# Kernel optimization log

Measured on AMD Instinct MI355X. Metric: run time of the kernel, lower is better.

## Reference

```python
import jax, jax.numpy as jnp
import numpy as np


def setup_inputs() -> dict:
    key = jax.random.key(0)
    ks = jax.random.split(key, 10)
    B, D_X, D_H, D_S, D_T = 16384, 256, 512, 128, 128
    G = 4 * D_H
    sc = lambda d: 1.0 / np.sqrt(d)
    return {
        "x": jax.random.normal(ks[0], (B, D_X), jnp.float32),
        "h": jax.random.normal(ks[1], (B, D_H), jnp.float32),
        "c": jax.random.normal(ks[2], (B, D_H), jnp.float32),
        "spatial_per_step": jax.random.normal(ks[3], (B, D_S), jnp.float32),
        "temporal_per_step": jax.random.normal(ks[4], (B, D_T), jnp.float32),
        "W_x": jax.random.normal(ks[5], (D_X, G), jnp.float32) * sc(D_X),
        "W_h": jax.random.normal(ks[6], (D_H, G), jnp.float32) * sc(D_H),
        "b_h": jax.random.normal(ks[7], (G,), jnp.float32) * 0.01,
        "W_s": jax.random.normal(ks[8], (D_S, G), jnp.float32) * sc(D_S),
        "W_t": jax.random.normal(ks[9], (D_T, G), jnp.float32) * sc(D_T),
    }


def reference(x, h, c, spatial_per_step, temporal_per_step, W_x, W_h, b_h, W_s, W_t):
    H = W_h.shape[0]  # hidden_size
    # Four gate projections summed (the fusion opportunity): [B, 4H]
    preact = (x @ W_x) + (h @ W_h + b_h) + (spatial_per_step @ W_s) + (temporal_per_step @ W_t)
    i_g = jax.nn.sigmoid(preact[:, 0 * H:1 * H])
    f_g = jax.nn.sigmoid(preact[:, 1 * H:2 * H])
    o_g = jax.nn.sigmoid(preact[:, 2 * H:3 * H])
    c_g = jnp.tanh(preact[:, 3 * H:4 * H])
    c_new = f_g * c + i_g * c_g
    # NOTE: faithful to the source, h = tanh(o * c) (not o * tanh(c))
    h_new = jnp.tanh(o_g * c_new)
    return (h_new, c_new)
```

## Files before the change

kernel.cpp:

```cpp
#include <hip/hip_runtime.h>
#include <hip/hip_bf16.h>
#include <cstdint>

#define B_DIM 16384
#define DX 256
#define DH 512
#define DS 128
#define DT 128
#define KDIM 1024
#define NDIM 2048
#define HOUT 512

#define NT 32
#define SLOT 4096

typedef __attribute__((ext_vector_type(8))) short short8;
typedef __attribute__((ext_vector_type(4))) float floatx4;

union bf16x8 {
  short8 v;
  __hip_bfloat16 b[8];
};

__device__ __forceinline__ float fast_sigmoid(float x) {
  return 1.f / (1.f + __expf(-x));
}
__device__ __forceinline__ float fast_tanh(float x) {
  float e = __expf(-2.f * x);
  return (1.f - e) / (1.f + e);
}


__global__ __launch_bounds__(256) void pack_AW(
    const float* __restrict__ x, const float* __restrict__ h,
    const float* __restrict__ s, const float* __restrict__ t,
    const float* __restrict__ Wx, const float* __restrict__ Wh,
    const float* __restrict__ Ws, const float* __restrict__ Wt,
    __hip_bfloat16* __restrict__ Ap, __hip_bfloat16* __restrict__ Wp) {
  const int bid = blockIdx.x;
  if (bid < B_DIM * KDIM / 8 / 256) {
    int tid = bid * 256 + threadIdx.x;
    int r = tid >> 7;
    int k = (tid & 127) * 8;
    const float* p;
    if (k < 768) {
      p = (k < 256) ? (x + (size_t)r * DX + k) : (h + (size_t)r * DH + (k - 256));
    } else {
      p = (k < 896) ? (s + (size_t)r * DS + (k - 768)) : (t + (size_t)r * DT + (k - 896));
    }
    floatx4 v0 = *(const floatx4*)p;
    floatx4 v1 = *(const floatx4*)(p + 4);
    bf16x8 o;
#pragma unroll
    for (int j = 0; j < 4; ++j) {
      o.b[j]     = __float2bfloat16(v0[j]);
      o.b[4 + j] = __float2bfloat16(v1[j]);
    }
    *(short8*)(Ap + (size_t)tid * 8) = o.v;
  } else {
    int tid = (bid - B_DIM * KDIM / 8 / 256) * 256 + threadIdx.x;
    int pcol = tid >> 7;
    int k0 = (tid & 127) * 8;
    int nblk = pcol >> 7, r7 = pcol & 127;
    int wn = r7 >> 6, g = (r7 >> 4) & 3, hl = r7 & 15;
    int col = g * 512 + nblk * 32 + wn * 16 + hl;
    const float* src; int kl;
    if (k0 < 256)      { src = Wx; kl = k0; }
    else if (k0 < 768) { src = Wh; kl = k0 - 256; }
    else if (k0 < 896) { src = Ws; kl = k0 - 768; }
    else               { src = Wt; kl = k0 - 896; }
    bf16x8 o;
#pragma unroll
    for (int rr = 0; rr < 8; ++rr)
      o.b[rr] = __float2bfloat16(src[(size_t)(kl + rr) * NDIM + col]);
    *(short8*)(Wp + (size_t)tid * 8) = o.v;
  }
}

#define GLD(src, dst)                                              \
  __builtin_amdgcn_global_load_lds(                                \
      (const __attribute__((address_space(1))) void*)(src),        \
      (__attribute__((address_space(3))) void*)(dst), 16, 0, 0)

__global__ __launch_bounds__(256, 3) void lstm_gemm(
    const __hip_bfloat16* __restrict__ Ap, const __hip_bfloat16* __restrict__ Wp,
    const float* __restrict__ bh, const float* __restrict__ c_in,
    float* __restrict__ out) {
  __shared__ unsigned short As[3 * SLOT];
  __shared__ unsigned short Bs[3 * SLOT];

  const int tid = threadIdx.x;
  const int lane = tid & 63;
  const int wid = tid >> 6;
  const int wm = wid & 1;
  const int wn = wid >> 1;
  const int q = lane >> 4;
  const int fr = lane & 15;

  const int bid = blockIdx.x;
  const int wg = (bid & 7) * 256 + (bid >> 3);
  const int mb = wg >> 4;
  const int nblk = wg & 15;
  const int m0 = mb * 128;

  int aOff[4], bOff[4];
#pragma unroll
  for (int m = 0; m < 4; ++m) {
    int row = wm * 64 + m * 16 + fr;
    aOff[m] = row * 32 + (q ^ ((row >> 1) & 3)) * 8;
  }
#pragma unroll
  for (int n = 0; n < 4; ++n) {
    int colc = wn * 64 + n * 16 + fr;
    bOff[n] = colc * 32 + (q ^ ((colc >> 1) & 3)) * 8;
  }

  const int c0 = wid * 2, c1 = c0 + 1;
  const int r0 = c0 * 16 + (lane >> 2), r1 = c1 * 16 + (lane >> 2);
  const int ql = lane & 3;
  const int q0 = ql ^ ((r0 >> 1) & 3);
  const int q1 = ql ^ ((r1 >> 1) & 3);
  const __hip_bfloat16* aP0 = Ap + (size_t)(m0 + r0) * KDIM + q0 * 8;
  const __hip_bfloat16* aP1 = Ap + (size_t)(m0 + r1) * KDIM + q1 * 8;
  const __hip_bfloat16* bP0 = Wp + (size_t)(nblk * 128 + r0) * KDIM + q0 * 8;
  const __hip_bfloat16* bP1 = Wp + (size_t)(nblk * 128 + r1) * KDIM + q1 * 8;
  const int dA0 = c0 * 512, dA1 = c1 * 512;

  floatx4 acc[4][4];
#pragma unroll
  for (int i = 0; i < 4; ++i)
#pragma unroll
    for (int j = 0; j < 4; ++j) acc[i][j] = (floatx4)0.f;

  GLD(aP0,      &As[dA0]);        GLD(aP1,      &As[dA1]);
  GLD(bP0,      &Bs[dA0]);        GLD(bP1,      &Bs[dA1]);
  GLD(aP0 + 32, &As[SLOT + dA0]); GLD(aP1 + 32, &As[SLOT + dA1]);
  GLD(bP0 + 32, &Bs[SLOT + dA0]); GLD(bP1 + 32, &Bs[SLOT + dA1]);
  asm volatile("s_waitcnt vmcnt(4)\n\ts_barrier" ::: "memory");

  int sR = 0;
  int sS = 2 * SLOT;

  for (int t = 0; t < NT; ++t) {
    const int ts = (t + 2 < NT) ? (t + 2) : (NT - 1);
    const int kO = ts * 32;

    GLD(aP0 + kO, &As[sS + dA0]);
    GLD(aP1 + kO, &As[sS + dA1]);
    GLD(bP0 + kO, &Bs[sS + dA0]);
    GLD(bP1 + kO, &Bs[sS + dA1]);

    short8 af[4], bf[4];
#pragma unroll
    for (int i = 0; i < 4; ++i) af[i] = *(const short8*)&As[sR + aOff[i]];
#pragma unroll
    for (int i = 0; i < 4; ++i) bf[i] = *(const short8*)&Bs[sR + bOff[i]];

    __builtin_amdgcn_s_setprio(1);
#pragma unroll
    for (int mi = 0; mi < 4; ++mi)
#pragma unroll
      for (int ni = 0; ni < 4; ++ni)
        acc[mi][ni] = __builtin_amdgcn_mfma_f32_16x16x32_bf16(
            af[mi], bf[ni], acc[mi][ni], 0, 0, 0);
    __builtin_amdgcn_s_setprio(0);

    asm volatile("s_waitcnt vmcnt(4)\n\ts_barrier" ::: "memory");

    sR = (sR == 2 * SLOT) ? 0 : sR + SLOT;
    sS = (sS == 2 * SLOT) ? 0 : sS + SLOT;
  }

  const int hh = nblk * 32 + wn * 16 + fr;
  float bias[4];
#pragma unroll
  for (int g = 0; g < 4; ++g) bias[g] = bh[g * 512 + hh];

#pragma unroll
  for (int mi = 0; mi < 4; ++mi) {
#pragma unroll
    for (int r = 0; r < 4; ++r) {
      const size_t grow = (size_t)(m0 + wm * 64 + mi * 16 + q * 4 + r);
      const float pi = acc[mi][0][r] + bias[0];
      const float pf = acc[mi][1][r] + bias[1];
      const float po = acc[mi][2][r] + bias[2];
      const float pc = acc[mi][3][r] + bias[3];
      const float ig = fast_sigmoid(pi);
      const float fg = fast_sigmoid(pf);
      const float og = fast_sigmoid(po);
      const float cg = fast_tanh(pc);
      const float cc = fg * c_in[grow * HOUT + hh] + ig * cg;
      out[grow * HOUT + hh] = fast_tanh(og * cc);
      out[(size_t)B_DIM * HOUT + grow * HOUT + hh] = cc;
    }
  }
}

extern "C" void kernel_launch(void* const* d_in, const int* in_sizes, int n_in,
                              void* d_out, int out_size, void* d_ws, size_t ws_size,
                              hipStream_t stream) {
  const float* x  = (const float*)d_in[0];
  const float* h  = (const float*)d_in[1];
  const float* c  = (const float*)d_in[2];
  const float* sp = (const float*)d_in[3];
  const float* tp = (const float*)d_in[4];
  const float* Wx = (const float*)d_in[5];
  const float* Wh = (const float*)d_in[6];
  const float* bh = (const float*)d_in[7];
  const float* Ws = (const float*)d_in[8];
  const float* Wt = (const float*)d_in[9];
  float* out = (float*)d_out;

  __hip_bfloat16* Ap = (__hip_bfloat16*)d_ws;
  __hip_bfloat16* Wp = (__hip_bfloat16*)((char*)d_ws + (size_t)B_DIM * KDIM * 2);

  const int nblk_A = B_DIM * KDIM / 8 / 256;
  const int nblk_W = NDIM * KDIM / 8 / 256;
  pack_AW<<<dim3(nblk_A + nblk_W), dim3(256), 0, stream>>>(
      x, h, sp, tp, Wx, Wh, Ws, Wt, Ap, Wp);
  lstm_gemm<<<dim3(2048), dim3(256), 0, stream>>>(Ap, Wp, bh, c, out);
}
```

Baseline: 263.4 us.

## Pre-tile packed operands into LDS-ready chunks and drop triple-buffered pipeline

After: 232.5 us. -11.7%, faster.

```diff
diff --git a/kernel.cpp b/kernel.cpp
--- a/kernel.cpp
+++ b/kernel.cpp
@@ -11,9 +11,6 @@
 #define NDIM 2048
 #define HOUT 512
 
-#define NT 32
-#define SLOT 4096
-
 typedef __attribute__((ext_vector_type(8))) short short8;
 typedef __attribute__((ext_vector_type(4))) float floatx4;
 
@@ -33,20 +30,29 @@
 
 __global__ __launch_bounds__(256) void pack_AW(
     const float* __restrict__ x, const float* __restrict__ h,
-    const float* __restrict__ s, const float* __restrict__ t,
+    const float* __restrict__ sp_, const float* __restrict__ tp_,
     const float* __restrict__ Wx, const float* __restrict__ Wh,
     const float* __restrict__ Ws, const float* __restrict__ Wt,
     __hip_bfloat16* __restrict__ Ap, __hip_bfloat16* __restrict__ Wp) {
+  const int NA = B_DIM * KDIM / 8 / 256;
   const int bid = blockIdx.x;
-  if (bid < B_DIM * KDIM / 8 / 256) {
+  if (bid < NA) {
     int tid = bid * 256 + threadIdx.x;
-    int r = tid >> 7;
-    int k = (tid & 127) * 8;
+    int i = tid & 63;
+    int t16 = (tid >> 6) & 15;
+    int tile = tid >> 10;
+    int kb = tile & 15, mb = tile >> 4;
+    int s = t16 >> 3, c = t16 & 7;
+    int row = c * 16 + (i >> 2);
+    int kq = (i & 3) ^ ((row >> 1) & 3);
+    int b = mb * 128 + row;
+    int k = kb * 64 + s * 32 + kq * 8;
     const float* p;
     if (k < 768) {
-      p = (k < 256) ? (x + (size_t)r * DX + k) : (h + (size_t)r * DH + (k - 256));
+      p = (k < 256) ? (x + (size_t)b * DX + k) : (h + (size_t)b * DH + (k - 256));
     } else {
-      p = (k < 896) ? (s + (size_t)r * DS + (k - 768)) : (t + (size_t)r * DT + (k - 896));
+      p = (k < 896) ? (sp_ + (size_t)b * DS + (k - 768))
+                    : (tp_ + (size_t)b * DT + (k - 896));
     }
     floatx4 v0 = *(const floatx4*)p;
     floatx4 v1 = *(const floatx4*)(p + 4);
@@ -58,21 +64,26 @@
     }
     *(short8*)(Ap + (size_t)tid * 8) = o.v;
   } else {
-    int tid = (bid - B_DIM * KDIM / 8 / 256) * 256 + threadIdx.x;
-    int pcol = tid >> 7;
-    int k0 = (tid & 127) * 8;
-    int nblk = pcol >> 7, r7 = pcol & 127;
-    int wn = r7 >> 6, g = (r7 >> 4) & 3, hl = r7 & 15;
+    int tid = (bid - NA) * 256 + threadIdx.x;
+    int i = tid & 63;
+    int t16 = (tid >> 6) & 15;
+    int tile = tid >> 10;
+    int kb = tile & 15, nblk = tile >> 4;
+    int s = t16 >> 3, c = t16 & 7;
+    int pcol = c * 16 + (i >> 2);
+    int kq = (i & 3) ^ ((pcol >> 1) & 3);
+    int k = kb * 64 + s * 32 + kq * 8;
+    int wn = pcol >> 6, g = (pcol >> 4) & 3, hl = pcol & 15;
     int col = g * 512 + nblk * 32 + wn * 16 + hl;
     const float* src; int kl;
-    if (k0 < 256)      { src = Wx; kl = k0; }
-    else if (k0 < 768) { src = Wh; kl = k0 - 256; }
-    else if (k0 < 896) { src = Ws; kl = k0 - 768; }
-    else               { src = Wt; kl = k0 - 896; }
+    if (k < 256)      { src = Wx; kl = k; }
+    else if (k < 768) { src = Wh; kl = k - 256; }
+    else if (k < 896) { src = Ws; kl = k - 768; }
+    else              { src = Wt; kl = k - 896; }
     bf16x8 o;
 #pragma unroll
-    for (int rr = 0; rr < 8; ++rr)
-      o.b[rr] = __float2bfloat16(src[(size_t)(kl + rr) * NDIM + col]);
+    for (int r = 0; r < 8; ++r)
+      o.b[r] = __float2bfloat16(src[(size_t)(kl + r) * NDIM + col]);
     *(short8*)(Wp + (size_t)tid * 8) = o.v;
   }
 }
@@ -86,8 +97,8 @@
     const __hip_bfloat16* __restrict__ Ap, const __hip_bfloat16* __restrict__ Wp,
     const float* __restrict__ bh, const float* __restrict__ c_in,
     float* __restrict__ out) {
-  __shared__ unsigned short As[3 * SLOT];
-  __shared__ unsigned short Bs[3 * SLOT];
+  __shared__ unsigned short As[8192];
+  __shared__ unsigned short Bs[8192];
 
   const int tid = threadIdx.x;
   const int lane = tid & 63;
@@ -115,60 +126,42 @@
     bOff[n] = colc * 32 + (q ^ ((colc >> 1) & 3)) * 8;
   }
 
-  const int c0 = wid * 2, c1 = c0 + 1;
-  const int r0 = c0 * 16 + (lane >> 2), r1 = c1 * 16 + (lane >> 2);
-  const int ql = lane & 3;
-  const int q0 = ql ^ ((r0 >> 1) & 3);
-  const int q1 = ql ^ ((r1 >> 1) & 3);
-  const __hip_bfloat16* aP0 = Ap + (size_t)(m0 + r0) * KDIM + q0 * 8;
-  const __hip_bfloat16* aP1 = Ap + (size_t)(m0 + r1) * KDIM + q1 * 8;
-  const __hip_bfloat16* bP0 = Wp + (size_t)(nblk * 128 + r0) * KDIM + q0 * 8;
-  const __hip_bfloat16* bP1 = Wp + (size_t)(nblk * 128 + r1) * KDIM + q1 * 8;
-  const int dA0 = c0 * 512, dA1 = c1 * 512;
-
   floatx4 acc[4][4];
 #pragma unroll
   for (int i = 0; i < 4; ++i)
 #pragma unroll
     for (int j = 0; j < 4; ++j) acc[i][j] = (floatx4)0.f;
 
-  GLD(aP0,      &As[dA0]);        GLD(aP1,      &As[dA1]);
-  GLD(bP0,      &Bs[dA0]);        GLD(bP1,      &Bs[dA1]);
-  GLD(aP0 + 32, &As[SLOT + dA0]); GLD(aP1 + 32, &As[SLOT + dA1]);
-  GLD(bP0 + 32, &Bs[SLOT + dA0]); GLD(bP1 + 32, &Bs[SLOT + dA1]);
-  asm volatile("s_waitcnt vmcnt(4)\n\ts_barrier" ::: "memory");
-
-  int sR = 0;
-  int sS = 2 * SLOT;
-
-  for (int t = 0; t < NT; ++t) {
-    const int ts = (t + 2 < NT) ? (t + 2) : (NT - 1);
-    const int kO = ts * 32;
-
-    GLD(aP0 + kO, &As[sS + dA0]);
-    GLD(aP1 + kO, &As[sS + dA1]);
-    GLD(bP0 + kO, &Bs[sS + dA0]);
-    GLD(bP1 + kO, &Bs[sS + dA1]);
-
-    short8 af[4], bf[4];
-#pragma unroll
-    for (int i = 0; i < 4; ++i) af[i] = *(const short8*)&As[sR + aOff[i]];
-#pragma unroll
-    for (int i = 0; i < 4; ++i) bf[i] = *(const short8*)&Bs[sR + bOff[i]];
-
-    __builtin_amdgcn_s_setprio(1);
-#pragma unroll
-    for (int mi = 0; mi < 4; ++mi)
-#pragma unroll
-      for (int ni = 0; ni < 4; ++ni)
-        acc[mi][ni] = __builtin_amdgcn_mfma_f32_16x16x32_bf16(
-            af[mi], bf[ni], acc[mi][ni], 0, 0, 0);
-    __builtin_amdgcn_s_setprio(0);
-
-    asm volatile("s_waitcnt vmcnt(4)\n\ts_barrier" ::: "memory");
-
-    sR = (sR == 2 * SLOT) ? 0 : sR + SLOT;
-    sS = (sS == 2 * SLOT) ? 0 : sS + SLOT;
+  const __hip_bfloat16* aTile = Ap + (size_t)(mb * 16) * 8192 + lane * 8;
+  const __hip_bfloat16* bTile = Wp + (size_t)(nblk * 16) * 8192 + lane * 8;
+
+  for (int kb = 0; kb < 16; ++kb) {
+    const __hip_bfloat16* ap = aTile + (size_t)kb * 8192;
+    const __hip_bfloat16* bp = bTile + (size_t)kb * 8192;
+#pragma unroll
+    for (int j = 0; j < 4; ++j) {
+      const int chunk = wid * 4 + j;
+      GLD(ap + chunk * 512, &As[chunk * 512]);
+      GLD(bp + chunk * 512, &Bs[chunk * 512]);
+    }
+    __syncthreads();
+
+#pragma unroll
+    for (int s = 0; s < 2; ++s) {
+      const int sb = s * 4096;
+      short8 af[4], bf[4];
+#pragma unroll
+      for (int i = 0; i < 4; ++i) af[i] = *(const short8*)&As[sb + aOff[i]];
+#pragma unroll
+      for (int i = 0; i < 4; ++i) bf[i] = *(const short8*)&Bs[sb + bOff[i]];
+#pragma unroll
+      for (int mi = 0; mi < 4; ++mi)
+#pragma unroll
+        for (int ni = 0; ni < 4; ++ni)
+          acc[mi][ni] = __builtin_amdgcn_mfma_f32_16x16x32_bf16(
+              af[mi], bf[ni], acc[mi][ni], 0, 0, 0);
+    }
+    __syncthreads();
   }
 
   const int hh = nblk * 32 + wn * 16 + fr;
```
